# Optimization experiments

Measured on AMD Instinct MI355X. Metric: run time of the kernel, lower is better.

The kernel has to match this reference:

```python
import jax, jax.numpy as jnp
import numpy as np

N = 20000      # nodes
E = 320000     # edges (no self loops; PyG adds them with fill_value='mean')
FIN = 16       # node feature dim
ED = 22        # edge feature dim
NEG_SLOPE = 0.2


def _lin(k, i, o):
    return (jax.random.normal(k, (i, o)) * (1.0 / np.sqrt(i))).astype(jnp.float32)


def setup_inputs() -> dict:
    key = jax.random.key(0)
    ks = jax.random.split(key, 32)
    x = jax.random.normal(ks[0], (N, FIN), dtype=jnp.float32)
    src = jax.random.randint(ks[1], (E,), 0, N, dtype=jnp.int32)
    off = jax.random.randint(ks[2], (E,), 1, N, dtype=jnp.int32)
    dst = (src + off) % N  # guarantees no pre-existing self loops
    edge_index = jnp.stack([src, dst], axis=0)
    edge_attr = jax.random.normal(ks[3], (E, ED), dtype=jnp.float32)

    def conv_params(kbase, fin, H, C):
        k = jax.random.split(kbase, 6)
        return dict(
            W=_lin(k[0], fin, H * C),
            att_s=jax.random.normal(k[1], (H, C), dtype=jnp.float32) * 0.1,
            att_d=jax.random.normal(k[2], (H, C), dtype=jnp.float32) * 0.1,
            We=_lin(k[3], ED, H * C),
            att_e=jax.random.normal(k[4], (H, C), dtype=jnp.float32) * 0.1,
            b=jnp.zeros((H * C,), dtype=jnp.float32),
        )

    p1 = conv_params(ks[4], FIN, 8, 32)
    p2 = conv_params(ks[5], 256, 8, 32)
    p3 = conv_params(ks[6], 256, 12, 64)
    Wf = _lin(ks[7], 256 + 256 + 768, 1)
    bf = jnp.zeros((1,), dtype=jnp.float32)
    return {
        'x': x, 'edge_index': edge_index, 'edge_attr': edge_attr,
        'W1': p1['W'], 'as1': p1['att_s'], 'ad1': p1['att_d'], 'We1': p1['We'], 'ae1': p1['att_e'], 'b1': p1['b'],
        'W2': p2['W'], 'as2': p2['att_s'], 'ad2': p2['att_d'], 'We2': p2['We'], 'ae2': p2['att_e'], 'b2': p2['b'],
        'W3': p3['W'], 'as3': p3['att_s'], 'ad3': p3['att_d'], 'We3': p3['We'], 'ae3': p3['att_e'], 'b3': p3['b'],
        'Wf': Wf, 'bf': bf,
    }


def _add_self_loops_mean(src, dst, edge_attr):
    # PyG add_self_loops(fill_value='mean'): self-loop edge_attr = mean of
    # incoming edge_attr at each node (0 for isolated nodes).
    cnt = jax.ops.segment_sum(jnp.ones((E,), jnp.float32), dst, N)  # [N]
    mean_ea = jax.ops.segment_sum(edge_attr, dst, N) / jnp.maximum(cnt, 1.0)[:, None]
    loop = jnp.arange(N, dtype=src.dtype)
    src_f = jnp.concatenate([src, loop])
    dst_f = jnp.concatenate([dst, loop])
    ea_f = jnp.concatenate([edge_attr, mean_ea], axis=0)
    return src_f, dst_f, ea_f


def _gat_conv(x, src, dst, ea, W, att_s, att_d, We, att_e, b, H, C):
    # node/edge projections
    h = (x @ W).reshape(-1, H, C)                  # [N,H,C]
    e = (ea @ We).reshape(-1, H, C)                # [E',H,C]
    a_s = jnp.sum(h * att_s, axis=-1)              # [N,H]
    a_d = jnp.sum(h * att_d, axis=-1)              # [N,H]
    a_e = jnp.sum(e * att_e, axis=-1)              # [E',H]
    alpha = a_s[src] + a_d[dst] + a_e              # [E',H]
    alpha = jax.nn.leaky_relu(alpha, NEG_SLOPE)
    # segment softmax over edges sharing a destination node
    amax = jax.ops.segment_max(alpha, dst, N)      # every node has a self loop
    ex = jnp.exp(alpha - amax[dst])
    denom = jax.ops.segment_sum(ex, dst, N)
    w = ex / denom[dst]                            # [E',H]
    out = jax.ops.segment_sum(w[:, :, None] * h[src], dst, N)  # [N,H,C]
    return out.reshape(-1, H * C) + b


def reference(x, edge_index, edge_attr,
              W1, as1, ad1, We1, ae1, b1,
              W2, as2, ad2, We2, ae2, b2,
              W3, as3, ad3, We3, ae3, b3,
              Wf, bf):
    src, dst = edge_index[0], edge_index[1]
    src_f, dst_f, ea_f = _add_self_loops_mean(src, dst, edge_attr)
    x1 = jax.nn.relu(_gat_conv(x, src_f, dst_f, ea_f, W1, as1, ad1, We1, ae1, b1, 8, 32))
    x2 = jax.nn.relu(_gat_conv(x1, src_f, dst_f, ea_f, W2, as2, ad2, We2, ae2, b2, 8, 32))
    x3 = jax.nn.relu(_gat_conv(x2, src_f, dst_f, ea_f, W3, as3, ad3, We3, ae3, b3, 12, 64))
    xc = jnp.concatenate([x1, x2, x3], axis=1)     # [N,1280]
    return jax.nn.sigmoid(xc @ Wf + bf)
```

## Files before the change

### kernel.cpp

```cpp
#include <hip/hip_runtime.h>

#define NN 20000
#define EE 320000
#define EF 340000
#define EDIM 22
#define NBLK ((NN + 255) / 256)

typedef short bf16x8 __attribute__((ext_vector_type(8)));
typedef float f32x4 __attribute__((ext_vector_type(4)));

__device__ __forceinline__ float blo(unsigned u) {
  union { unsigned x; float f; } v; v.x = u << 16; return v.f;
}
__device__ __forceinline__ float bhi(unsigned u) {
  union { unsigned x; float f; } v; v.x = u & 0xffff0000u; return v.f;
}
__device__ __forceinline__ ushort f2b(float f) {
  union { float f; unsigned u; } v;
  v.f = f;
  unsigned u = v.u;
  return (ushort)((u + 0x7fffu + ((u >> 16) & 1u)) >> 16);
}
__device__ __forceinline__ float lrelu(float a) { return a > 0.f ? a : 0.2f * a; }


__global__ void count_deg_kernel(const int* __restrict__ dst, int* __restrict__ cnt) {
  int e = blockIdx.x * blockDim.x + threadIdx.x;
  if (e < EE) atomicAdd(&cnt[dst[e]], 1);
}

__global__ void scan1_kernel(const int* __restrict__ cnt, int* __restrict__ off,
                             int* __restrict__ btot) {
  __shared__ int wsum[4];
  const int b = blockIdx.x, tid = threadIdx.x;
  const int lane = tid & 63, w = tid >> 6;
  const int i = b * 256 + tid;
  int v = (i < NN) ? (cnt[i] + 1) : 0;
  int x = v;
#pragma unroll
  for (int s = 1; s < 64; s <<= 1) {
    int t = __shfl_up(x, s);
    if (lane >= s) x += t;
  }
  if (lane == 63) wsum[w] = x;
  __syncthreads();
  if (tid == 0) {
    int a = 0;
#pragma unroll
    for (int k = 0; k < 4; ++k) { int t = wsum[k]; wsum[k] = a; a += t; }
  }
  __syncthreads();
  int excl = wsum[w] + x - v;
  if (i < NN) off[i] = excl;
  if (tid == 255) btot[b] = wsum[3] + x;
}

__global__ void scan2_kernel(int* __restrict__ btot) {
  __shared__ int s0;
  const int tid = threadIdx.x, lane = tid & 63, w = tid >> 6;
  int v = (tid < NBLK) ? btot[tid] : 0;
  int x = v;
#pragma unroll
  for (int s = 1; s < 64; s <<= 1) {
    int t = __shfl_up(x, s);
    if (lane >= s) x += t;
  }
  if (w == 0 && lane == 63) s0 = x;
  __syncthreads();
  int excl = x - v + (w ? s0 : 0);
  if (tid < NBLK) btot[tid] = excl;
}

__global__ void scan3_kernel(int* __restrict__ off, const int* __restrict__ btot,
                             int* __restrict__ cursor) {
  const int i = blockIdx.x * blockDim.x + threadIdx.x;
  if (i < NN) {
    int o = off[i] + btot[i >> 8];
    off[i] = o;
    cursor[i] = o;
  }
  if (i == 0) off[NN] = EF;
}

__global__ void scatter_kernel(const int* __restrict__ src, const int* __restrict__ dst,
                               int* __restrict__ cursor, int* __restrict__ csr_src,
                               int* __restrict__ csr_dst, int* __restrict__ csr_eid) {
  int e = blockIdx.x * blockDim.x + threadIdx.x;
  if (e >= EF) return;
  int s, d;
  if (e < EE) { s = src[e]; d = dst[e]; } else { s = e - EE; d = s; }
  int pos = atomicAdd(&cursor[d], 1);
  csr_src[pos] = s;
  csr_dst[pos] = d;
  csr_eid[pos] = e;
}

__global__ __launch_bounds__(256) void mean_ea_kernel(
    const int* __restrict__ off, const int* __restrict__ csr_eid,
    const float* __restrict__ edge_attr, float* __restrict__ mean_ea) {
  const int n = (int)((blockIdx.x * blockDim.x + threadIdx.x) >> 6);
  const int lane = threadIdx.x & 63;
  if (n >= NN) return;
  const int start = off[n], end = off[n + 1];
  float a[24];
#pragma unroll
  for (int d = 0; d < 24; ++d) a[d] = 0.f;
  for (int j = start + lane; j < end; j += 64) {
    int eid = csr_eid[j];
    if (eid < EE) {
      const float* ea = edge_attr + (size_t)eid * EDIM;
      float4 q0 = *(const float4*)(ea + 0);
      float4 q1 = *(const float4*)(ea + 4);
      float4 q2 = *(const float4*)(ea + 8);
      float4 q3 = *(const float4*)(ea + 12);
      float4 q4 = *(const float4*)(ea + 16);
      float2 q5 = *(const float2*)(ea + 20);
      a[0] += q0.x; a[1] += q0.y; a[2] += q0.z; a[3] += q0.w;
      a[4] += q1.x; a[5] += q1.y; a[6] += q1.z; a[7] += q1.w;
      a[8] += q2.x; a[9] += q2.y; a[10] += q2.z; a[11] += q2.w;
      a[12] += q3.x; a[13] += q3.y; a[14] += q3.z; a[15] += q3.w;
      a[16] += q4.x; a[17] += q4.y; a[18] += q4.z; a[19] += q4.w;
      a[20] += q5.x; a[21] += q5.y;
    }
  }
#pragma unroll
  for (int s = 32; s > 0; s >>= 1)
#pragma unroll
    for (int d = 0; d < EDIM; ++d) a[d] += __shfl_xor(a[d], s);
  if (lane == 0) {
    const float den = 1.f / fmaxf((float)(end - start - 1), 1.f);
    float* mp = mean_ea + (size_t)n * EDIM;
#pragma unroll
    for (int d = 0; d < EDIM; ++d) mp[d] = a[d] * den;
  }
}


__global__ void cvt_x_kernel(const float* __restrict__ x, ushort* __restrict__ ab) {
  int t = blockIdx.x * blockDim.x + threadIdx.x;
  if (t >= NN * 32) return;
  int n = t >> 5, c = t & 31;
  ab[t] = (c < 16) ? f2b(x[n * 16 + c]) : (ushort)0;
}

__global__ void prep_weights_kernel(
    const float* __restrict__ W1, const float* __restrict__ W2, const float* __restrict__ W3,
    ushort* __restrict__ wt1, ushort* __restrict__ wt2, ushort* __restrict__ wt3,
    const float* __restrict__ We1, const float* __restrict__ ate1, float* __restrict__ wec1,
    const float* __restrict__ We2, const float* __restrict__ ate2, float* __restrict__ wec2,
    const float* __restrict__ We3, const float* __restrict__ ate3, float* __restrict__ wec3) {
  int t = blockIdx.x * blockDim.x + threadIdx.x;
  const int S0 = 256 * 32, S1 = 256 * 256, S2 = 768 * 256;
  const int S3 = EDIM * 8, S4 = EDIM * 8, S5 = EDIM * 12;
  if (t < S0) {
    int nc = t >> 5, k = t & 31;
    wt1[t] = (k < 16) ? f2b(W1[(size_t)k * 256 + nc]) : (ushort)0;
    return;
  }
  t -= S0;
  if (t < S1) {
    int nc = t >> 8, k = t & 255;
    wt2[t] = f2b(W2[(size_t)k * 256 + nc]);
    return;
  }
  t -= S1;
  if (t < S2) {
    int nc = t >> 8, k = t & 255;
    wt3[t] = f2b(W3[(size_t)k * 768 + nc]);
    return;
  }
  t -= S2;
  if (t < S3) {
    int d = t / 8, h = t % 8;
    float v = 0.f;
    for (int c = 0; c < 32; ++c) v += We1[(size_t)d * 256 + h * 32 + c] * ate1[h * 32 + c];
    wec1[t] = v;
    return;
  }
  t -= S3;
  if (t < S4) {
    int d = t / 8, h = t % 8;
    float v = 0.f;
    for (int c = 0; c < 32; ++c) v += We2[(size_t)d * 256 + h * 32 + c] * ate2[h * 32 + c];
    wec2[t] = v;
    return;
  }
  t -= S4;
  if (t < S5) {
    int d = t / 12, h = t % 12;
    float v = 0.f;
    for (int c = 0; c < 64; ++c) v += We3[(size_t)d * 768 + h * 64 + c] * ate3[h * 64 + c];
    wec3[t] = v;
  }
}

template <int K, int CDIM>
__global__ __launch_bounds__(256) void gemm_lds_kernel(
    const ushort* __restrict__ A, const ushort* __restrict__ Bt,
    ushort* __restrict__ C, const float* __restrict__ atts,
    const float* __restrict__ attd, float* __restrict__ a_s,
    float* __restrict__ a_d, int M, int Nc, int H) {
  constexpr int CPC = K / 8;
  constexpr int SWZ = (CPC - 1) < 7 ? (CPC - 1) : 7;
  __shared__ __align__(16) ushort Blds[64 * K];
  const int tid = threadIdx.x;
  const int lane = tid & 63;
  const int wid = tid >> 6;
  const int bn = blockIdx.x * 64;
  const int bm = blockIdx.y * 128 + wid * 32;
  const int r = lane & 15;
  const int kg = lane >> 4;

#pragma unroll
  for (int it = 0; it < (64 * CPC) / 256; ++it) {
    int idx = it * 256 + tid;
    int col = idx / CPC;
    int c = idx % CPC;
    const uint4 v = *(const uint4*)(Bt + (size_t)(bn + col) * K + c * 8);
    *(uint4*)(&Blds[(col * CPC + (c ^ (col & SWZ))) * 8]) = v;
  }
  __syncthreads();

  const int row0 = bm + r, row1 = bm + 16 + r;
  const bool v0 = row0 < M, v1 = row1 < M;
  const ushort* ap0 = A + (size_t)row0 * K + kg * 8;
  const ushort* ap1 = A + (size_t)row1 * K + kg * 8;

  f32x4 acc[2][4] = {};
#pragma unroll
  for (int k0 = 0; k0 < K; k0 += 32) {
    bf16x8 a0 = {}, a1 = {};
    if (v0) a0 = *(const bf16x8*)(ap0 + k0);
    if (v1) a1 = *(const bf16x8*)(ap1 + k0);
    const int cbase = k0 / 8 + kg;
#pragma unroll
    for (int nf = 0; nf < 4; ++nf) {
      const int col = nf * 16 + r;
      bf16x8 bfr = *(const bf16x8*)(&Blds[(col * CPC + (cbase ^ (col & SWZ))) * 8]);
      acc[0][nf] = __builtin_amdgcn_mfma_f32_16x16x32_bf16(a0, bfr, acc[0][nf], 0, 0, 0);
      acc[1][nf] = __builtin_amdgcn_mfma_f32_16x16x32_bf16(a1, bfr, acc[1][nf], 0, 0, 0);
    }
  }
#pragma unroll
  for (int half = 0; half < 2; ++half)
#pragma unroll
    for (int nf = 0; nf < 4; ++nf)
#pragma unroll
      for (int reg = 0; reg < 4; ++reg) {
        int row = bm + half * 16 + kg * 4 + reg;
        if (row < M) C[(size_t)row * Nc + bn + nf * 16 + r] = f2b(acc[half][nf][reg]);
      }

  float as_v[4], ad_v[4];
#pragma unroll
  for (int nf = 0; nf < 4; ++nf) {
    int cg = bn + nf * 16 + r;
    as_v[nf] = atts[cg];
    ad_v[nf] = attd[cg];
  }
  const int h0g = bn / CDIM;
#pragma unroll
  for (int half = 0; half < 2; ++half) {
#pragma unroll
    for (int reg = 0; reg < 4; ++reg) {
      float sA, dA, sB = 0.f, dB = 0.f;
      if (CDIM == 32) {
        sA = acc[half][0][reg] * as_v[0] + acc[half][1][reg] * as_v[1];
        dA = acc[half][0][reg] * ad_v[0] + acc[half][1][reg] * ad_v[1];
        sB = acc[half][2][reg] * as_v[2] + acc[half][3][reg] * as_v[3];
        dB = acc[half][2][reg] * ad_v[2] + acc[half][3][reg] * ad_v[3];
      } else {
        sA = acc[half][0][reg] * as_v[0] + acc[half][1][reg] * as_v[1] +
             acc[half][2][reg] * as_v[2] + acc[half][3][reg] * as_v[3];
        dA = acc[half][0][reg] * ad_v[0] + acc[half][1][reg] * ad_v[1] +
             acc[half][2][reg] * ad_v[2] + acc[half][3][reg] * ad_v[3];
      }
#pragma unroll
      for (int s = 8; s >= 1; s >>= 1) {
        sA += __shfl_xor(sA, s);
        dA += __shfl_xor(dA, s);
        if (CDIM == 32) { sB += __shfl_xor(sB, s); dB += __shfl_xor(dB, s); }
      }
      if (r == 0) {
        int row = bm + half * 16 + kg * 4 + reg;
        if (row < M) {
          a_s[row * H + h0g] = sA;
          a_d[row * H + h0g] = dA;
          if (CDIM == 32) {
            a_s[row * H + h0g + 1] = sB;
            a_d[row * H + h0g + 1] = dB;
          }
        }
      }
    }
  }
}

__global__ void ase_kernel(const int* __restrict__ csr_eid, const int* __restrict__ csr_src,
                           const int* __restrict__ csr_dst,
                           const float* __restrict__ edge_attr, const float* __restrict__ mean_ea,
                           const float* __restrict__ wec, const float* __restrict__ a_s,
                           const float* __restrict__ a_d, float* __restrict__ wexp, int H) {
  int t = blockIdx.x * blockDim.x + threadIdx.x;
  if (t >= EF * H) return;
  int j = t / H, hh = t % H;
  int eid = csr_eid[j];
  const float* ea = (eid < EE) ? &edge_attr[(size_t)eid * EDIM]
                               : &mean_ea[(size_t)(eid - EE) * EDIM];
  float v = 0.f;
#pragma unroll
  for (int d = 0; d < EDIM; ++d) v += ea[d] * wec[d * H + hh];
  v += a_s[csr_src[j] * H + hh] + a_d[csr_dst[j] * H + hh];
  wexp[t] = __expf(lrelu(v));
}

template <int H, int C, int NCH>
__global__ __launch_bounds__(256) void aggregate_kernel(
    const float* __restrict__ wexp, const ushort* __restrict__ hb,
    const int* __restrict__ off, const int* __restrict__ csr_src,
    const float* __restrict__ bias, ushort* __restrict__ xb) {
  constexpr int HC = H * C;
  constexpr int CHUNK = HC / NCH;
  constexpr int FPL = CHUNK / 64;
  const int t = (int)((blockIdx.x * blockDim.x + threadIdx.x) >> 6);
  const int lane = threadIdx.x & 63;
  const int n = t / NCH, ch = t - n * NCH;
  if (n >= NN) return;
  const int start = off[n], end = off[n + 1];
  const int f0 = ch * CHUNK + lane * FPL;
  const int qh = f0 / C;
  const ushort* hrow = hb + f0;
  const float* wp = wexp + qh;

  float acc[FPL] = {};
  float dn = 0.f;
  int j = start;
  for (; j + 4 <= end; j += 4) {
    int s0 = csr_src[j], s1 = csr_src[j + 1], s2 = csr_src[j + 2], s3 = csr_src[j + 3];
    float w0 = wp[(size_t)j * H];
    float w1 = wp[(size_t)(j + 1) * H];
    float w2 = wp[(size_t)(j + 2) * H];
    float w3 = wp[(size_t)(j + 3) * H];
    uint2 u0 = *(const uint2*)(hrow + (size_t)s0 * HC);
    uint2 u1 = *(const uint2*)(hrow + (size_t)s1 * HC);
    uint2 u2 = *(const uint2*)(hrow + (size_t)s2 * HC);
    uint2 u3 = *(const uint2*)(hrow + (size_t)s3 * HC);
    dn += (w0 + w1) + (w2 + w3);
    acc[0] += w0 * blo(u0.x) + w1 * blo(u1.x) + w2 * blo(u2.x) + w3 * blo(u3.x);
    acc[1] += w0 * bhi(u0.x) + w1 * bhi(u1.x) + w2 * bhi(u2.x) + w3 * bhi(u3.x);
    acc[2] += w0 * blo(u0.y) + w1 * blo(u1.y) + w2 * blo(u2.y) + w3 * blo(u3.y);
    acc[3] += w0 * bhi(u0.y) + w1 * bhi(u1.y) + w2 * bhi(u2.y) + w3 * bhi(u3.y);
  }
  for (; j < end; ++j) {
    int s0 = csr_src[j];
    float w0 = wp[(size_t)j * H];
    uint2 u0 = *(const uint2*)(hrow + (size_t)s0 * HC);
    dn += w0;
    acc[0] += w0 * blo(u0.x);
    acc[1] += w0 * bhi(u0.x);
    acc[2] += w0 * blo(u0.y);
    acc[3] += w0 * bhi(u0.y);
  }

  const float my_rd = 1.f / dn;
  ushort o[FPL];
#pragma unroll
  for (int i = 0; i < FPL; ++i) o[i] = f2b(fmaxf(acc[i] * my_rd + bias[f0 + i], 0.f));
  uint2 pk;
  pk.x = (unsigned)o[0] | ((unsigned)o[1] << 16);
  pk.y = (unsigned)o[2] | ((unsigned)o[3] << 16);
  *(uint2*)(xb + (size_t)n * HC + f0) = pk;
}

__global__ void final_kernel(const ushort* __restrict__ x1b, const ushort* __restrict__ x2b,
                             const ushort* __restrict__ x3b, const float* __restrict__ Wf,
                             const float* __restrict__ bf, float* __restrict__ out) {
  const int wave = (int)((blockIdx.x * blockDim.x + threadIdx.x) >> 6);
  const int lane = threadIdx.x & 63;
  if (wave >= NN) return;
  float acc = 0.f;
#pragma unroll
  for (int q = 0; q < 5; ++q) {
    int f0 = (q * 64 + lane) * 4;
    const ushort* sp;
    if (f0 < 256)      sp = x1b + (size_t)wave * 256 + f0;
    else if (f0 < 512) sp = x2b + (size_t)wave * 256 + (f0 - 256);
    else               sp = x3b + (size_t)wave * 768 + (f0 - 512);
    uint2 u = *(const uint2*)sp;
    float4 wv = *(const float4*)(Wf + f0);
    acc += blo(u.x) * wv.x + bhi(u.x) * wv.y + blo(u.y) * wv.z + bhi(u.y) * wv.w;
  }
#pragma unroll
  for (int s = 32; s > 0; s >>= 1) acc += __shfl_xor(acc, s);
  if (lane == 0) out[wave] = 1.f / (1.f + __expf(-(acc + bf[0])));
}


extern "C" void kernel_launch(void* const* d_in, const int* in_sizes, int n_in,
                              void* d_out, int out_size, void* d_ws, size_t ws_size,
                              hipStream_t stream) {
  const float* x     = (const float*)d_in[0];
  const int*   eidx  = (const int*)d_in[1];
  const float* eattr = (const float*)d_in[2];
  const float* W[3]   = {(const float*)d_in[3],  (const float*)d_in[9],  (const float*)d_in[15]};
  const float* ats[3] = {(const float*)d_in[4],  (const float*)d_in[10], (const float*)d_in[16]};
  const float* atd[3] = {(const float*)d_in[5],  (const float*)d_in[11], (const float*)d_in[17]};
  const float* We[3]  = {(const float*)d_in[6],  (const float*)d_in[12], (const float*)d_in[18]};
  const float* ate[3] = {(const float*)d_in[7],  (const float*)d_in[13], (const float*)d_in[19]};
  const float* bb[3]  = {(const float*)d_in[8],  (const float*)d_in[14], (const float*)d_in[20]};
  const float* Wf = (const float*)d_in[21];
  const float* bf = (const float*)d_in[22];
  float* out = (float*)d_out;

  const int* src = eidx;
  const int* dst = eidx + EE;

  char* p = (char*)d_ws;
  auto carve = [&](size_t bytes) -> char* {
    char* q = p;
    p += (bytes + 255) & ~(size_t)255;
    return q;
  };
  ushort* x1b   = (ushort*)carve((size_t)NN * 256 * 2);
  ushort* x2b   = (ushort*)carve((size_t)NN * 256 * 2);
  ushort* x3b   = (ushort*)carve((size_t)NN * 768 * 2);
  ushort* hbuf  = (ushort*)carve((size_t)NN * 768 * 2);
  ushort* abf1  = (ushort*)carve((size_t)NN * 32 * 2);
  ushort* wt1   = (ushort*)carve((size_t)256 * 32 * 2);
  ushort* wt2   = (ushort*)carve((size_t)256 * 256 * 2);
  ushort* wt3   = (ushort*)carve((size_t)768 * 256 * 2);
  float*  a_s   = (float*)carve((size_t)NN * 12 * 4);
  float*  a_d   = (float*)carve((size_t)NN * 12 * 4);
  float*  wexp  = (float*)carve((size_t)EF * 12 * 4);
  float*  mea   = (float*)carve((size_t)NN * EDIM * 4);
  float*  wec1  = (float*)carve((size_t)EDIM * 8 * 4);
  float*  wec2  = (float*)carve((size_t)EDIM * 8 * 4);
  float*  wec3  = (float*)carve((size_t)EDIM * 12 * 4);
  int* cnt      = (int*)carve((size_t)NN * 4);
  int* off      = (int*)carve((size_t)(NN + 1) * 4);
  int* btot     = (int*)carve((size_t)NBLK * 4);
  int* cursor   = (int*)carve((size_t)NN * 4);
  int* csr_src  = (int*)carve((size_t)EF * 4);
  int* csr_dst  = (int*)carve((size_t)EF * 4);
  int* csr_eid  = (int*)carve((size_t)EF * 4);

  hipMemsetAsync(cnt, 0, (size_t)NN * 4, stream);
  count_deg_kernel<<<(EE + 255) / 256, 256, 0, stream>>>(dst, cnt);
  scan1_kernel<<<NBLK, 256, 0, stream>>>(cnt, off, btot);
  scan2_kernel<<<1, 128, 0, stream>>>(btot);
  scan3_kernel<<<NBLK, 256, 0, stream>>>(off, btot, cursor);
  scatter_kernel<<<(EF + 255) / 256, 256, 0, stream>>>(src, dst, cursor, csr_src, csr_dst,
                                                       csr_eid);
  mean_ea_kernel<<<(NN * 64 + 255) / 256, 256, 0, stream>>>(off, csr_eid, eattr, mea);

  cvt_x_kernel<<<(NN * 32 + 255) / 256, 256, 0, stream>>>(x, abf1);
  {
    const int total = 256 * 32 + 256 * 256 + 768 * 256 + EDIM * 8 + EDIM * 8 + EDIM * 12;
    prep_weights_kernel<<<(total + 255) / 256, 256, 0, stream>>>(
        W[0], W[1], W[2], wt1, wt2, wt3,
        We[0], ate[0], wec1, We[1], ate[1], wec2, We[2], ate[2], wec3);
  }

  const int Hs[3] = {8, 8, 12};
  const ushort* Ain[3] = {abf1, x1b, x2b};
  const ushort* Wt[3] = {wt1, wt2, wt3};
  float* wecL[3] = {wec1, wec2, wec3};
  ushort* xoutb[3] = {x1b, x2b, x3b};

  for (int L = 0; L < 3; ++L) {
    const int H = Hs[L];
    const int HC = (L < 2) ? 256 : 768;
    dim3 g(HC / 64, (NN + 127) / 128);
    if (L == 0)
      gemm_lds_kernel<32, 32><<<g, 256, 0, stream>>>(Ain[L], Wt[L], hbuf, ats[L], atd[L],
                                                     a_s, a_d, NN, HC, H);
    else if (L == 1)
      gemm_lds_kernel<256, 32><<<g, 256, 0, stream>>>(Ain[L], Wt[L], hbuf, ats[L], atd[L],
                                                      a_s, a_d, NN, HC, H);
    else
      gemm_lds_kernel<256, 64><<<g, 256, 0, stream>>>(Ain[L], Wt[L], hbuf, ats[L], atd[L],
                                                      a_s, a_d, NN, HC, H);
    ase_kernel<<<(EF * H + 255) / 256, 256, 0, stream>>>(csr_eid, csr_src, csr_dst, eattr,
                                                         mea, wecL[L], a_s, a_d, wexp, H);
    if (H == 8) {
      int blocks = (NN * 1 + 3) / 4;
      aggregate_kernel<8, 32, 1><<<blocks, 256, 0, stream>>>(wexp, hbuf, off, csr_src,
                                                             bb[L], xoutb[L]);
    } else {
      int blocks = (NN * 3 + 3) / 4;
      aggregate_kernel<12, 64, 3><<<blocks, 256, 0, stream>>>(wexp, hbuf, off, csr_src,
                                                              bb[L], xoutb[L]);
    }
  }

  final_kernel<<<(NN * 64 + 255) / 256, 256, 0, stream>>>(x1b, x2b, x3b, Wf, bf, out);
}
```

Before: 347.6 us.

## Fuse final linear into aggregation and precompute bf16 CSR-ordered edge attributes

Each aggregate kernel now computes its partial dot product with the final weight vector and writes per-node logit partials. Layer 3 therefore no longer materialises its 768-wide output, and the final kernel shrinks to summing five partials and applying a sigmoid. Separately, edge attributes are gathered once into CSR order as bf16, so the three ase passes read contiguous half-size data instead of doing indirect fp32 gathers. This costs an extra kernel plus an extra buffer, and bf16 rounding of edge attributes changes numerics slightly.

```diff
diff --git a/kernel.cpp b/kernel.cpp
--- a/kernel.cpp
+++ b/kernel.cpp
@@ -135,6 +135,21 @@
   }
 }
 
+__global__ void ea_csr_kernel(const int* __restrict__ csr_eid,
+                              const float* __restrict__ edge_attr,
+                              const float* __restrict__ mean_ea,
+                              ushort* __restrict__ ea_csr) {
+  int t = blockIdx.x * blockDim.x + threadIdx.x;
+  if (t >= EF * 11) return;
+  int j = t / 11, dp = t % 11;
+  int eid = csr_eid[j];
+  const float* ea = (eid < EE) ? edge_attr + (size_t)eid * EDIM
+                               : mean_ea + (size_t)(eid - EE) * EDIM;
+  float2 v = *(const float2*)(ea + dp * 2);
+  unsigned u = (unsigned)f2b(v.x) | ((unsigned)f2b(v.y) << 16);
+  *(unsigned*)(ea_csr + (size_t)j * EDIM + dp * 2) = u;
+}
+
 
 __global__ void cvt_x_kernel(const float* __restrict__ x, ushort* __restrict__ ab) {
   int t = blockIdx.x * blockDim.x + threadIdx.x;
@@ -296,29 +311,30 @@
   }
 }
 
-__global__ void ase_kernel(const int* __restrict__ csr_eid, const int* __restrict__ csr_src,
-                           const int* __restrict__ csr_dst,
-                           const float* __restrict__ edge_attr, const float* __restrict__ mean_ea,
-                           const float* __restrict__ wec, const float* __restrict__ a_s,
-                           const float* __restrict__ a_d, float* __restrict__ wexp, int H) {
+__global__ void ase_kernel(const int* __restrict__ csr_src, const int* __restrict__ csr_dst,
+                           const ushort* __restrict__ ea_csr, const float* __restrict__ wec,
+                           const float* __restrict__ a_s, const float* __restrict__ a_d,
+                           float* __restrict__ wexp, int H) {
   int t = blockIdx.x * blockDim.x + threadIdx.x;
   if (t >= EF * H) return;
   int j = t / H, hh = t % H;
-  int eid = csr_eid[j];
-  const float* ea = (eid < EE) ? &edge_attr[(size_t)eid * EDIM]
-                               : &mean_ea[(size_t)(eid - EE) * EDIM];
+  const ushort* ea = ea_csr + (size_t)j * EDIM;
   float v = 0.f;
 #pragma unroll
-  for (int d = 0; d < EDIM; ++d) v += ea[d] * wec[d * H + hh];
+  for (int d = 0; d < 11; ++d) {
+    unsigned u = *(const unsigned*)(ea + 2 * d);
+    v += blo(u) * wec[(2 * d) * H + hh] + bhi(u) * wec[(2 * d + 1) * H + hh];
+  }
   v += a_s[csr_src[j] * H + hh] + a_d[csr_dst[j] * H + hh];
   wexp[t] = __expf(lrelu(v));
 }
 
-template <int H, int C, int NCH>
+template <int H, int C, int NCH, bool WRITE_X>
 __global__ __launch_bounds__(256) void aggregate_kernel(
     const float* __restrict__ wexp, const ushort* __restrict__ hb,
     const int* __restrict__ off, const int* __restrict__ csr_src,
-    const float* __restrict__ bias, ushort* __restrict__ xb) {
+    const float* __restrict__ bias, ushort* __restrict__ xb,
+    const float* __restrict__ WfL, float* __restrict__ logitpart, int slotbase) {
   constexpr int HC = H * C;
   constexpr int CHUNK = HC / NCH;
   constexpr int FPL = CHUNK / 64;
@@ -363,36 +379,34 @@
   }
 
   const float my_rd = 1.f / dn;
-  ushort o[FPL];
-#pragma unroll
-  for (int i = 0; i < FPL; ++i) o[i] = f2b(fmaxf(acc[i] * my_rd + bias[f0 + i], 0.f));
-  uint2 pk;
-  pk.x = (unsigned)o[0] | ((unsigned)o[1] << 16);
-  pk.y = (unsigned)o[2] | ((unsigned)o[3] << 16);
-  *(uint2*)(xb + (size_t)n * HC + f0) = pk;
-}
-
-__global__ void final_kernel(const ushort* __restrict__ x1b, const ushort* __restrict__ x2b,
-                             const ushort* __restrict__ x3b, const float* __restrict__ Wf,
-                             const float* __restrict__ bf, float* __restrict__ out) {
-  const int wave = (int)((blockIdx.x * blockDim.x + threadIdx.x) >> 6);
-  const int lane = threadIdx.x & 63;
-  if (wave >= NN) return;
-  float acc = 0.f;
-#pragma unroll
-  for (int q = 0; q < 5; ++q) {
-    int f0 = (q * 64 + lane) * 4;
-    const ushort* sp;
-    if (f0 < 256)      sp = x1b + (size_t)wave * 256 + f0;
-    else if (f0 < 512) sp = x2b + (size_t)wave * 256 + (f0 - 256);
-    else               sp = x3b + (size_t)wave * 768 + (f0 - 512);
-    uint2 u = *(const uint2*)sp;
-    float4 wv = *(const float4*)(Wf + f0);
-    acc += blo(u.x) * wv.x + bhi(u.x) * wv.y + blo(u.y) * wv.z + bhi(u.y) * wv.w;
-  }
-#pragma unroll
-  for (int s = 32; s > 0; s >>= 1) acc += __shfl_xor(acc, s);
-  if (lane == 0) out[wave] = 1.f / (1.f + __expf(-(acc + bf[0])));
+  const float4 wf4 = *(const float4*)(WfL + f0);
+  const float wfv[4] = {wf4.x, wf4.y, wf4.z, wf4.w};
+  float o[FPL];
+  float partial = 0.f;
+#pragma unroll
+  for (int i = 0; i < FPL; ++i) {
+    o[i] = fmaxf(acc[i] * my_rd + bias[f0 + i], 0.f);
+    partial += o[i] * wfv[i];
+  }
+  if (WRITE_X) {
+    uint2 pk;
+    pk.x = (unsigned)f2b(o[0]) | ((unsigned)f2b(o[1]) << 16);
+    pk.y = (unsigned)f2b(o[2]) | ((unsigned)f2b(o[3]) << 16);
+    *(uint2*)(xb + (size_t)n * HC + f0) = pk;
+  }
+#pragma unroll
+  for (int s = 32; s > 0; s >>= 1) partial += __shfl_xor(partial, s);
+  if (lane == 0) logitpart[n * 5 + slotbase + ch] = partial;
+}
+
+__global__ void final_sigmoid_kernel(const float* __restrict__ logitpart,
+                                     const float* __restrict__ bf,
+                                     float* __restrict__ out) {
+  int n = blockIdx.x * blockDim.x + threadIdx.x;
+  if (n >= NN) return;
+  const float* lp = logitpart + n * 5;
+  float s = lp[0] + lp[1] + lp[2] + lp[3] + lp[4] + bf[0];
+  out[n] = 1.f / (1.f + __expf(-s));
 }
 
 
@@ -421,28 +435,29 @@
     p += (bytes + 255) & ~(size_t)255;
     return q;
   };
-  ushort* x1b   = (ushort*)carve((size_t)NN * 256 * 2);
-  ushort* x2b   = (ushort*)carve((size_t)NN * 256 * 2);
-  ushort* x3b   = (ushort*)carve((size_t)NN * 768 * 2);
-  ushort* hbuf  = (ushort*)carve((size_t)NN * 768 * 2);
-  ushort* abf1  = (ushort*)carve((size_t)NN * 32 * 2);
-  ushort* wt1   = (ushort*)carve((size_t)256 * 32 * 2);
-  ushort* wt2   = (ushort*)carve((size_t)256 * 256 * 2);
-  ushort* wt3   = (ushort*)carve((size_t)768 * 256 * 2);
-  float*  a_s   = (float*)carve((size_t)NN * 12 * 4);
-  float*  a_d   = (float*)carve((size_t)NN * 12 * 4);
-  float*  wexp  = (float*)carve((size_t)EF * 12 * 4);
-  float*  mea   = (float*)carve((size_t)NN * EDIM * 4);
-  float*  wec1  = (float*)carve((size_t)EDIM * 8 * 4);
-  float*  wec2  = (float*)carve((size_t)EDIM * 8 * 4);
-  float*  wec3  = (float*)carve((size_t)EDIM * 12 * 4);
-  int* cnt      = (int*)carve((size_t)NN * 4);
-  int* off      = (int*)carve((size_t)(NN + 1) * 4);
-  int* btot     = (int*)carve((size_t)NBLK * 4);
-  int* cursor   = (int*)carve((size_t)NN * 4);
-  int* csr_src  = (int*)carve((size_t)EF * 4);
-  int* csr_dst  = (int*)carve((size_t)EF * 4);
-  int* csr_eid  = (int*)carve((size_t)EF * 4);
+  ushort* x1b    = (ushort*)carve((size_t)NN * 256 * 2);
+  ushort* x2b    = (ushort*)carve((size_t)NN * 256 * 2);
+  ushort* hbuf   = (ushort*)carve((size_t)NN * 768 * 2);
+  ushort* abf1   = (ushort*)carve((size_t)NN * 32 * 2);
+  ushort* wt1    = (ushort*)carve((size_t)256 * 32 * 2);
+  ushort* wt2    = (ushort*)carve((size_t)256 * 256 * 2);
+  ushort* wt3    = (ushort*)carve((size_t)768 * 256 * 2);
+  ushort* ea_csr = (ushort*)carve((size_t)EF * EDIM * 2);
+  float*  a_s    = (float*)carve((size_t)NN * 12 * 4);
+  float*  a_d    = (float*)carve((size_t)NN * 12 * 4);
+  float*  wexp   = (float*)carve((size_t)EF * 12 * 4);
+  float*  mea    = (float*)carve((size_t)NN * EDIM * 4);
+  float*  wec1   = (float*)carve((size_t)EDIM * 8 * 4);
+  float*  wec2   = (float*)carve((size_t)EDIM * 8 * 4);
+  float*  wec3   = (float*)carve((size_t)EDIM * 12 * 4);
+  float*  lpart  = (float*)carve((size_t)NN * 5 * 4);
+  int* cnt       = (int*)carve((size_t)NN * 4);
+  int* off       = (int*)carve((size_t)(NN + 1) * 4);
+  int* btot      = (int*)carve((size_t)NBLK * 4);
+  int* cursor    = (int*)carve((size_t)NN * 4);
+  int* csr_src   = (int*)carve((size_t)EF * 4);
+  int* csr_dst   = (int*)carve((size_t)EF * 4);
+  int* csr_eid   = (int*)carve((size_t)EF * 4);
 
   hipMemsetAsync(cnt, 0, (size_t)NN * 4, stream);
   count_deg_kernel<<<(EE + 255) / 256, 256, 0, stream>>>(dst, cnt);
@@ -452,6 +467,7 @@
   scatter_kernel<<<(EF + 255) / 256, 256, 0, stream>>>(src, dst, cursor, csr_src, csr_dst,
                                                        csr_eid);
   mean_ea_kernel<<<(NN * 64 + 255) / 256, 256, 0, stream>>>(off, csr_eid, eattr, mea);
+  ea_csr_kernel<<<(EF * 11 + 255) / 256, 256, 0, stream>>>(csr_eid, eattr, mea, ea_csr);
 
   cvt_x_kernel<<<(NN * 32 + 255) / 256, 256, 0, stream>>>(x, abf1);
   {
@@ -465,7 +481,9 @@
   const ushort* Ain[3] = {abf1, x1b, x2b};
   const ushort* Wt[3] = {wt1, wt2, wt3};
   float* wecL[3] = {wec1, wec2, wec3};
-  ushort* xoutb[3] = {x1b, x2b, x3b};
+  ushort* xoutb[3] = {x1b, x2b, nullptr};
+  const float* WfL[3] = {Wf, Wf + 256, Wf + 512};
+  const int slotb[3] = {0, 1, 2};
 
   for (int L = 0; L < 3; ++L) {
     const int H = Hs[L];
@@ -480,18 +498,18 @@
     else
       gemm_lds_kernel<256, 64><<<g, 256, 0, stream>>>(Ain[L], Wt[L], hbuf, ats[L], atd[L],
                                                       a_s, a_d, NN, HC, H);
-    ase_kernel<<<(EF * H + 255) / 256, 256, 0, stream>>>(csr_eid, csr_src, csr_dst, eattr,
-                                                         mea, wecL[L], a_s, a_d, wexp, H);
+    ase_kernel<<<(EF * H + 255) / 256, 256, 0, stream>>>(csr_src, csr_dst, ea_csr, wecL[L],
+                                                         a_s, a_d, wexp, H);
     if (H == 8) {
       int blocks = (NN * 1 + 3) / 4;
-      aggregate_kernel<8, 32, 1><<<blocks, 256, 0, stream>>>(wexp, hbuf, off, csr_src,
-                                                             bb[L], xoutb[L]);
+      aggregate_kernel<8, 32, 1, true><<<blocks, 256, 0, stream>>>(
+          wexp, hbuf, off, csr_src, bb[L], xoutb[L], WfL[L], lpart, slotb[L]);
     } else {
       int blocks = (NN * 3 + 3) / 4;
-      aggregate_kernel<12, 64, 3><<<blocks, 256, 0, stream>>>(wexp, hbuf, off, csr_src,
-                                                              bb[L], xoutb[L]);
+      aggregate_kernel<12, 64, 3, false><<<blocks, 256, 0, stream>>>(
+          wexp, hbuf, off, csr_src, bb[L], xoutb[L], WfL[L], lpart, slotb[L]);
     }
   }
 
-  final_kernel<<<(NN * 64 + 255) / 256, 256, 0, stream>>>(x1b, x2b, x3b, Wf, bf, out);
-}
+  final_sigmoid_kernel<<<(NN + 255) / 256, 256, 0, stream>>>(lpart, bf, out);
+}
```

New measurement: 342.1 us. Within noise of the previous version (-1.6%).
